# Kernel optimization log

Hardware: AMD Instinct MI355X
Metric: run time of the kernel (lower is better)

Reference implementation:

```python
import jax, jax.numpy as jnp
import numpy as np

B, M, D = 4, 2048, 1024


def setup_inputs() -> dict:
    key = jax.random.key(0)
    k1, k2, k3, k4 = jax.random.split(key, 4)
    x = jax.random.normal(k1, (B, M, D), dtype=jnp.float32)
    scale = 0.02
    wq = jax.random.normal(k2, (D, D), dtype=jnp.float32) * scale
    wk = jax.random.normal(k3, (D, D), dtype=jnp.float32) * scale
    wv = jax.random.normal(k4, (D, D), dtype=jnp.float32) * scale
    return {"x": x, "wq": wq, "wk": wk, "wv": wv}


def _rope_tables(m, d):
    # Faithful to source: phi = 10000 ** (-2*(i-1)/d)  (note the (i-1), incl. i=0)
    i = jnp.arange(d // 2, dtype=jnp.float32)
    phi = jnp.power(10000.0, -2.0 * (i - 1.0) / d)  # [d/2]
    pos = jnp.arange(m, dtype=jnp.float32)
    ang = pos[:, None] * phi[None, :]  # [m, d/2]
    return jnp.cos(ang), jnp.sin(ang)


def _apply_rope(t, cos, sin):
    # Original does t[pos] @ R[pos] (row-vector times rotation matrix):
    #   out_even =  t_even*cos + t_odd*sin
    #   out_odd  = -t_even*sin + t_odd*cos
    te = t[..., 0::2]  # [b, m, d/2]
    to = t[..., 1::2]
    oe = te * cos + to * sin
    oo = -te * sin + to * cos
    return jnp.stack([oe, oo], axis=-1).reshape(t.shape)


def reference(x, wq, wk, wv):
    b, m, d = x.shape
    q = x @ wq.T
    k = x @ wk.T
    v = x @ wv.T
    cos, sin = _rope_tables(m, d)
    qr = _apply_rope(q, cos, sin)
    kr = _apply_rope(k, cos, sin)
    # causal SDPA (dropout disabled for deterministic reference)
    scores = jnp.einsum('bqd,bkd->bqk', qr, kr) / jnp.sqrt(jnp.float32(d))
    causal = jnp.tril(jnp.ones((m, m), dtype=bool))
    scores = jnp.where(causal[None, :, :], scores, jnp.finfo(scores.dtype).min)
    attn = jax.nn.softmax(scores, axis=-1)
    return jnp.einsum('bqk,bkd->bqd', attn, v)
```

## Files before the change

### kernel.cpp

```cpp
#include <hip/hip_runtime.h>
#include <hip/hip_bf16.h>
#include <math.h>


typedef __bf16 bf16x8 __attribute__((ext_vector_type(8)));
typedef float  f32x4  __attribute__((ext_vector_type(4)));

__device__ __forceinline__ ushort f2bf(float f) {
    __hip_bfloat16 h = __float2bfloat16(f);
    return *reinterpret_cast<ushort*>(&h);
}

__device__ __forceinline__ void async_load16(const ushort* g, ushort* l) {
    __builtin_amdgcn_global_load_lds(
        (const __attribute__((address_space(1))) void*)g,
        (__attribute__((address_space(3))) void*)l, 16, 0, 0);
}

__global__ __launch_bounds__(256) void cvt_all_kernel(
    const float* __restrict__ x,  const float* __restrict__ wq,
    const float* __restrict__ wk, const float* __restrict__ wv,
    ushort* __restrict__ xb, ushort* __restrict__ wqb,
    ushort* __restrict__ wkb, ushort* __restrict__ wvb,
    float2* __restrict__ cs)
{
    const int t = blockIdx.y;
    if (t == 4) {
        const int idx = blockIdx.x * 256 + threadIdx.x;
        if (idx < 2048 * 512) {
            const int pos = idx >> 9, i = idx & 511;
            const float phi = powf(10000.0f, -2.0f * ((float)i - 1.0f) / 1024.0f);
            float s, c;
            sincosf((float)pos * phi, &s, &c);
            cs[idx] = make_float2(c, s);
        }
        return;
    }
    const float* in  = (t == 0) ? x  : (t == 1) ? wq  : (t == 2) ? wk  : wv;
    ushort*      out = (t == 0) ? xb : (t == 1) ? wqb : (t == 2) ? wkb : wvb;
    const int n4 = (t == 0) ? 2097152 : 262144;
    int i = blockIdx.x * blockDim.x + threadIdx.x;
    if (i < n4) {
        float4 f = ((const float4*)in)[i];
        ushort4 o;
        o.x = f2bf(f.x); o.y = f2bf(f.y); o.z = f2bf(f.z); o.w = f2bf(f.w);
        ((ushort4*)out)[i] = o;
    }
}

__device__ __forceinline__ void gemm128_core_sb64(
    const ushort* __restrict__ A, const ushort* __restrict__ B,
    int lda, int ldb, int m0, int n0, int kIters,
    ushort* As, ushort* Bs, f32x4 acc[4][4])
{
    const int tid  = threadIdx.x;
    const int lane = tid & 63, wave = tid >> 6;
    const int wm = (wave >> 1) * 64, wn = (wave & 1) * 64;
    const int quad = lane >> 4, l16 = lane & 15;
    const int srow8 = lane >> 3;
    const int gchk  = (lane & 7) ^ srow8;
    const ushort* ag = A + (size_t)(m0 + wave * 32 + srow8) * lda + gchk * 8;
    const ushort* bg = B + (size_t)(n0 + wave * 32 + srow8) * ldb + gchk * 8;
    const int p0 = quad ^ (l16 & 7);

    for (int kt = 0; kt < kIters; ++kt) {
        const int k0 = kt * 64;
#pragma unroll
        for (int s = 0; s < 4; ++s) {
            async_load16(ag + k0 + (size_t)(s * 8) * lda,
                         As + (wave * 32 + s * 8) * 64);
            async_load16(bg + k0 + (size_t)(s * 8) * ldb,
                         Bs + (wave * 32 + s * 8) * 64);
        }
        __syncthreads();
#pragma unroll
        for (int kk = 0; kk < 2; ++kk) {
            const int poff = (p0 ^ (kk << 2)) * 8;
            bf16x8 aF[4], bF[4];
#pragma unroll
            for (int i = 0; i < 4; ++i)
                aF[i] = *(const bf16x8*)(As + (wm + i * 16 + l16) * 64 + poff);
#pragma unroll
            for (int j = 0; j < 4; ++j)
                bF[j] = *(const bf16x8*)(Bs + (wn + j * 16 + l16) * 64 + poff);
#pragma unroll
            for (int i = 0; i < 4; ++i)
#pragma unroll
                for (int j = 0; j < 4; ++j)
                    acc[i][j] = __builtin_amdgcn_mfma_f32_16x16x32_bf16(aF[i], bF[j], acc[i][j], 0, 0, 0);
        }
        __syncthreads();
    }
}

__device__ __forceinline__ void gemm128_core_db64(
    const ushort* __restrict__ A, const ushort* __restrict__ B,
    int lda, int ldb, int m0, int n0, int kIters,
    ushort* As, ushort* Bs, f32x4 acc[4][4])
{
    const int tid  = threadIdx.x;
    const int lane = tid & 63, wave = tid >> 6;
    const int wm = (wave >> 1) * 64, wn = (wave & 1) * 64;
    const int quad = lane >> 4, l16 = lane & 15;
    const int srow8 = lane >> 3;
    const int gchk  = (lane & 7) ^ srow8;
    const ushort* ag = A + (size_t)(m0 + wave * 32 + srow8) * lda + gchk * 8;
    const ushort* bg = B + (size_t)(n0 + wave * 32 + srow8) * ldb + gchk * 8;
    const int p0 = quad ^ (l16 & 7);

#define STAGE64(K0, NB) do {                                            \
        _Pragma("unroll")                                               \
        for (int s = 0; s < 4; ++s) {                                   \
            async_load16(ag + (K0) + (size_t)(s * 8) * lda,             \
                         As + (NB) + (wave * 32 + s * 8) * 64);         \
            async_load16(bg + (K0) + (size_t)(s * 8) * ldb,             \
                         Bs + (NB) + (wave * 32 + s * 8) * 64);         \
        }                                                               \
    } while (0)

    STAGE64(0, 0);
    __syncthreads();

    int cur = 0;
    for (int kt = 0; kt < kIters; ++kt) {
        if (kt + 1 < kIters) STAGE64((kt + 1) * 64, (cur ^ 1) * 8192);
        const ushort* as = As + cur * 8192;
        const ushort* bs = Bs + cur * 8192;
#pragma unroll
        for (int kk = 0; kk < 2; ++kk) {
            const int poff = (p0 ^ (kk << 2)) * 8;
            bf16x8 aF[4], bF[4];
#pragma unroll
            for (int i = 0; i < 4; ++i)
                aF[i] = *(const bf16x8*)(as + (wm + i * 16 + l16) * 64 + poff);
#pragma unroll
            for (int j = 0; j < 4; ++j)
                bF[j] = *(const bf16x8*)(bs + (wn + j * 16 + l16) * 64 + poff);
#pragma unroll
            for (int i = 0; i < 4; ++i)
#pragma unroll
                for (int j = 0; j < 4; ++j)
                    acc[i][j] = __builtin_amdgcn_mfma_f32_16x16x32_bf16(aF[i], bF[j], acc[i][j], 0, 0, 0);
        }
        __syncthreads();
        cur ^= 1;
    }
#undef STAGE64
}

#define ACC_INIT4(acc) \
    _Pragma("unroll") for (int i = 0; i < 4; ++i) \
    _Pragma("unroll") for (int j = 0; j < 4; ++j) \
    _Pragma("unroll") for (int r = 0; r < 4; ++r) acc[i][j][r] = 0.0f;

__global__ __launch_bounds__(256) void qkv_rope_kernel(
    const ushort* __restrict__ xb, const ushort* __restrict__ wq,
    const ushort* __restrict__ wk, const ushort* __restrict__ wv,
    const float2* __restrict__ cs,
    ushort* __restrict__ Qr, ushort* __restrict__ Kr, ushort* __restrict__ VT)
{
    __shared__ __attribute__((aligned(16))) ushort As[128 * 64];
    __shared__ __attribute__((aligned(16))) ushort Bs[128 * 64];
    const int m0 = blockIdx.x * 128;
    const int n0 = blockIdx.y * 128;
    const int z  = blockIdx.z;
    const ushort* W = (z == 0) ? wq : (z == 1) ? wk : wv;

    f32x4 acc[4][4];
    ACC_INIT4(acc)
    gemm128_core_sb64(xb, W, 1024, 1024, m0, n0, 16, As, Bs, acc);

    const int lane = threadIdx.x & 63, wave = threadIdx.x >> 6;
    const int wm = (wave >> 1) * 64, wn = (wave & 1) * 64;
    const int quad = lane >> 4, l16 = lane & 15;

    if (z < 2) {
        ushort* out = (z == 0) ? Qr : Kr;
#pragma unroll
        for (int j = 0; j < 4; ++j) {
            const int n = n0 + wn + j * 16 + l16;
            const int iidx = n >> 1;
            const bool odd = n & 1;
#pragma unroll
            for (int i = 0; i < 4; ++i) {
                const int mbase = m0 + wm + i * 16 + quad * 4;
                const int pos0  = mbase & 2047;
                const float2* csp = cs + (size_t)pos0 * 512 + iidx;
#pragma unroll
                for (int r = 0; r < 4; ++r) {
                    const float2 sc = csp[(size_t)r * 512];
                    float v = acc[i][j][r];
                    float p = __shfl_xor(v, 1);
                    float o = odd ? (v * sc.x - p * sc.y) : (v * sc.x + p * sc.y);
                    out[(size_t)(mbase + r) * 1024 + n] = f2bf(o);
                }
            }
        }
    } else {
#pragma unroll
        for (int i = 0; i < 4; ++i) {
            const int mbase = m0 + wm + i * 16 + quad * 4;
            const int b = mbase >> 11, pos0 = mbase & 2047;
#pragma unroll
            for (int j = 0; j < 4; ++j) {
                const int n = n0 + wn + j * 16 + l16;
                ushort4 o;
                o.x = f2bf(acc[i][j][0]); o.y = f2bf(acc[i][j][1]);
                o.z = f2bf(acc[i][j][2]); o.w = f2bf(acc[i][j][3]);
                *(ushort4*)(VT + ((size_t)b * 1024 + n) * 2048 + pos0) = o;
            }
        }
    }
}

__global__ __launch_bounds__(256) void scores_kernel(
    const ushort* __restrict__ Qr, const ushort* __restrict__ Kr,
    float* __restrict__ S)
{
    const int m0 = blockIdx.x * 128;
    const int n0 = blockIdx.y * 128;
    if (n0 > m0 + 127) return;
    const int b = blockIdx.z;
    __shared__ __attribute__((aligned(16))) ushort As[2 * 128 * 64];
    __shared__ __attribute__((aligned(16))) ushort Bs[2 * 128 * 64];
    const ushort* A = Qr + (size_t)b * 2048 * 1024;
    const ushort* B = Kr + (size_t)b * 2048 * 1024;
    float* Sb = S + (size_t)b * 2048 * 2048;

    f32x4 acc[4][4];
    ACC_INIT4(acc)
    gemm128_core_db64(A, B, 1024, 1024, m0, n0, 16, As, Bs, acc);

    const int lane = threadIdx.x & 63, wave = threadIdx.x >> 6;
    const int wm = (wave >> 1) * 64, wn = (wave & 1) * 64;
    const int quad = lane >> 4, l16 = lane & 15;
#pragma unroll
    for (int i = 0; i < 4; ++i)
#pragma unroll
        for (int j = 0; j < 4; ++j) {
            const int n = n0 + wn + j * 16 + l16;
#pragma unroll
            for (int r = 0; r < 4; ++r) {
                const int m = m0 + wm + i * 16 + quad * 4 + r;
                Sb[(size_t)m * 2048 + n] = acc[i][j][r] * 0.03125f;
            }
        }
}

__global__ __launch_bounds__(256) void softmax_kernel(
    const float* __restrict__ S, ushort* __restrict__ P)
{
    __shared__ float red[4];
    const int row = blockIdx.x, tid = threadIdx.x, b = blockIdx.y;
    const int lane = tid & 63, wave = tid >> 6;
    const float* s = S + ((size_t)b * 2048 + row) * 2048;
    ushort*      p = P + ((size_t)b * 2048 + row) * 2048;
    const int nvalid = row + 1;
    const int wlimit = (row & ~127) + 128;
    const int j0 = tid * 8;

    float v[8] = {0.0f, 0.0f, 0.0f, 0.0f, 0.0f, 0.0f, 0.0f, 0.0f};
    if (j0 < nvalid) {
        float4 f0 = *(const float4*)(s + j0);
        v[0]=f0.x; v[1]=f0.y; v[2]=f0.z; v[3]=f0.w;
    }
    if (j0 + 4 < nvalid) {
        float4 f1 = *(const float4*)(s + j0 + 4);
        v[4]=f1.x; v[5]=f1.y; v[6]=f1.z; v[7]=f1.w;
    }

    float mx = -3.402823466e38f;
#pragma unroll
    for (int u = 0; u < 8; ++u) if (j0 + u < nvalid) mx = fmaxf(mx, v[u]);
#pragma unroll
    for (int d = 1; d < 64; d <<= 1) mx = fmaxf(mx, __shfl_xor(mx, d));
    if (lane == 0) red[wave] = mx;
    __syncthreads();
    mx = fmaxf(fmaxf(red[0], red[1]), fmaxf(red[2], red[3]));

    float sum = 0.0f;
#pragma unroll
    for (int u = 0; u < 8; ++u) {
        v[u] = (j0 + u < nvalid) ? __expf(v[u] - mx) : 0.0f;
        sum += v[u];
    }
#pragma unroll
    for (int d = 1; d < 64; d <<= 1) sum += __shfl_xor(sum, d);
    __syncthreads();
    if (lane == 0) red[wave] = sum;
    __syncthreads();
    const float inv = 1.0f / (red[0] + red[1] + red[2] + red[3]);

    if (j0 < wlimit) {
        ushort o[8];
#pragma unroll
        for (int u = 0; u < 8; ++u) o[u] = f2bf(v[u] * inv);
        *(int4*)(p + j0) = *(const int4*)o;
    }
}

__global__ __launch_bounds__(256) void pv_kernel(
    const ushort* __restrict__ P, const ushort* __restrict__ VT,
    float* __restrict__ out)
{
    __shared__ __attribute__((aligned(16))) ushort As[2 * 128 * 64];
    __shared__ __attribute__((aligned(16))) ushort Bs[2 * 128 * 64];
    const int x  = blockIdx.x;
    const int mt = (x & 1) ? (15 - (x >> 1)) : (x >> 1);
    const int m0 = mt * 128;
    const int n0 = blockIdx.y * 128;
    const int b  = blockIdx.z;
    const ushort* A = P + (size_t)b * 2048 * 2048;
    const ushort* B = VT + (size_t)b * 1024 * 2048;
    const int kIters = (m0 + 128) / 64;

    f32x4 acc[4][4];
    ACC_INIT4(acc)
    gemm128_core_db64(A, B, 2048, 2048, m0, n0, kIters, As, Bs, acc);

    const int lane = threadIdx.x & 63, wave = threadIdx.x >> 6;
    const int wm = (wave >> 1) * 64, wn = (wave & 1) * 64;
    const int quad = lane >> 4, l16 = lane & 15;
#pragma unroll
    for (int i = 0; i < 4; ++i)
#pragma unroll
        for (int j = 0; j < 4; ++j) {
            const int n = n0 + wn + j * 16 + l16;
#pragma unroll
            for (int r = 0; r < 4; ++r) {
                const int m = m0 + wm + i * 16 + quad * 4 + r;
                out[((size_t)b * 2048 + m) * 1024 + n] = acc[i][j][r];
            }
        }
}

extern "C" void kernel_launch(void* const* d_in, const int* in_sizes, int n_in,
                              void* d_out, int out_size, void* d_ws, size_t ws_size,
                              hipStream_t stream) {
    const float* x  = (const float*)d_in[0];
    const float* wq = (const float*)d_in[1];
    const float* wk = (const float*)d_in[2];
    const float* wv = (const float*)d_in[3];

    const size_t MiB = 1024 * 1024;
    char* ws = (char*)d_ws;
    ushort* xb  = (ushort*)(ws);
    ushort* wqb = (ushort*)(ws +  16 * MiB);
    ushort* wkb = (ushort*)(ws +  18 * MiB);
    ushort* wvb = (ushort*)(ws +  20 * MiB);
    ushort* Qr  = (ushort*)(ws +  22 * MiB);
    ushort* Kr  = (ushort*)(ws +  38 * MiB);
    ushort* VT  = (ushort*)(ws +  54 * MiB);
    float*  S   = (float* )(ws +  70 * MiB);
    ushort* P   = (ushort*)(ws + 134 * MiB);
    float2* cs  = (float2*)(ws + 166 * MiB);
    float*  out = (float*)d_out;

    cvt_all_kernel <<<dim3(8192, 5),   256, 0, stream>>>(x, wq, wk, wv, xb, wqb, wkb, wvb, cs);
    qkv_rope_kernel<<<dim3(64, 8, 3),  256, 0, stream>>>(xb, wqb, wkb, wvb, cs, Qr, Kr, VT);
    scores_kernel  <<<dim3(16, 16, 4), 256, 0, stream>>>(Qr, Kr, S);
    softmax_kernel <<<dim3(2048, 4),   256, 0, stream>>>(S, P);
    pv_kernel      <<<dim3(16, 8, 4),  256, 0, stream>>>(P, VT, out);
}
```

Before: 258.5 us.

## Enlarge QKV projection tile to 256x256 with 512-thread blocks

Rewrites the QKV+RoPE projection GEMM to use 256x256 output tiles computed by 8 waves, each holding a 128x64 sub-tile (8x4 MFMA accumulators), instead of 128x128 tiles with 4 waves. This raises arithmetic intensity per LDS load and cuts global re-reads of x and the weights. The grid drops from 1536 to 384 blocks, which may underfill the GPU's CUs, and doubled accumulator registers plus 64KB LDS lower occupancy. The unused single-buffer helper is removed.

```diff
diff --git a/kernel.cpp b/kernel.cpp
--- a/kernel.cpp
+++ b/kernel.cpp
@@ -48,7 +48,7 @@
     }
 }
 
-__device__ __forceinline__ void gemm128_core_sb64(
+__device__ __forceinline__ void gemm128_core_db64(
     const ushort* __restrict__ A, const ushort* __restrict__ B,
     int lda, int ldb, int m0, int n0, int kIters,
     ushort* As, ushort* Bs, f32x4 acc[4][4])
@@ -63,51 +63,6 @@
     const ushort* bg = B + (size_t)(n0 + wave * 32 + srow8) * ldb + gchk * 8;
     const int p0 = quad ^ (l16 & 7);
 
-    for (int kt = 0; kt < kIters; ++kt) {
-        const int k0 = kt * 64;
-#pragma unroll
-        for (int s = 0; s < 4; ++s) {
-            async_load16(ag + k0 + (size_t)(s * 8) * lda,
-                         As + (wave * 32 + s * 8) * 64);
-            async_load16(bg + k0 + (size_t)(s * 8) * ldb,
-                         Bs + (wave * 32 + s * 8) * 64);
-        }
-        __syncthreads();
-#pragma unroll
-        for (int kk = 0; kk < 2; ++kk) {
-            const int poff = (p0 ^ (kk << 2)) * 8;
-            bf16x8 aF[4], bF[4];
-#pragma unroll
-            for (int i = 0; i < 4; ++i)
-                aF[i] = *(const bf16x8*)(As + (wm + i * 16 + l16) * 64 + poff);
-#pragma unroll
-            for (int j = 0; j < 4; ++j)
-                bF[j] = *(const bf16x8*)(Bs + (wn + j * 16 + l16) * 64 + poff);
-#pragma unroll
-            for (int i = 0; i < 4; ++i)
-#pragma unroll
-                for (int j = 0; j < 4; ++j)
-                    acc[i][j] = __builtin_amdgcn_mfma_f32_16x16x32_bf16(aF[i], bF[j], acc[i][j], 0, 0, 0);
-        }
-        __syncthreads();
-    }
-}
-
-__device__ __forceinline__ void gemm128_core_db64(
-    const ushort* __restrict__ A, const ushort* __restrict__ B,
-    int lda, int ldb, int m0, int n0, int kIters,
-    ushort* As, ushort* Bs, f32x4 acc[4][4])
-{
-    const int tid  = threadIdx.x;
-    const int lane = tid & 63, wave = tid >> 6;
-    const int wm = (wave >> 1) * 64, wn = (wave & 1) * 64;
-    const int quad = lane >> 4, l16 = lane & 15;
-    const int srow8 = lane >> 3;
-    const int gchk  = (lane & 7) ^ srow8;
-    const ushort* ag = A + (size_t)(m0 + wave * 32 + srow8) * lda + gchk * 8;
-    const ushort* bg = B + (size_t)(n0 + wave * 32 + srow8) * ldb + gchk * 8;
-    const int p0 = quad ^ (l16 & 7);
-
 #define STAGE64(K0, NB) do {                                            \
         _Pragma("unroll")                                               \
         for (int s = 0; s < 4; ++s) {                                   \
@@ -153,26 +108,66 @@
     _Pragma("unroll") for (int j = 0; j < 4; ++j) \
     _Pragma("unroll") for (int r = 0; r < 4; ++r) acc[i][j][r] = 0.0f;
 
-__global__ __launch_bounds__(256) void qkv_rope_kernel(
+__global__ __launch_bounds__(512) void qkv_rope_kernel(
     const ushort* __restrict__ xb, const ushort* __restrict__ wq,
     const ushort* __restrict__ wk, const ushort* __restrict__ wv,
     const float2* __restrict__ cs,
     ushort* __restrict__ Qr, ushort* __restrict__ Kr, ushort* __restrict__ VT)
 {
-    __shared__ __attribute__((aligned(16))) ushort As[128 * 64];
-    __shared__ __attribute__((aligned(16))) ushort Bs[128 * 64];
-    const int m0 = blockIdx.x * 128;
-    const int n0 = blockIdx.y * 128;
+    __shared__ __attribute__((aligned(16))) ushort As[256 * 64];
+    __shared__ __attribute__((aligned(16))) ushort Bs[256 * 64];
+    const int m0 = blockIdx.x * 256;
+    const int n0 = blockIdx.y * 256;
     const int z  = blockIdx.z;
     const ushort* W = (z == 0) ? wq : (z == 1) ? wk : wv;
 
-    f32x4 acc[4][4];
-    ACC_INIT4(acc)
-    gemm128_core_sb64(xb, W, 1024, 1024, m0, n0, 16, As, Bs, acc);
-
-    const int lane = threadIdx.x & 63, wave = threadIdx.x >> 6;
-    const int wm = (wave >> 1) * 64, wn = (wave & 1) * 64;
+    const int tid  = threadIdx.x;
+    const int lane = tid & 63, wave = tid >> 6;
+    const int wm = (wave >> 2) * 128;
+    const int wn = (wave & 3) * 64;
     const int quad = lane >> 4, l16 = lane & 15;
+    const int srow8 = lane >> 3;
+    const int gchk  = (lane & 7) ^ srow8;
+    const ushort* ag = xb + (size_t)(m0 + wave * 32 + srow8) * 1024 + gchk * 8;
+    const ushort* bg = W  + (size_t)(n0 + wave * 32 + srow8) * 1024 + gchk * 8;
+    const int p0 = quad ^ (l16 & 7);
+
+    f32x4 acc[8][4];
+#pragma unroll
+    for (int i = 0; i < 8; ++i)
+#pragma unroll
+        for (int j = 0; j < 4; ++j)
+#pragma unroll
+            for (int r = 0; r < 4; ++r) acc[i][j][r] = 0.0f;
+
+    for (int kt = 0; kt < 16; ++kt) {
+        const int k0 = kt * 64;
+#pragma unroll
+        for (int s = 0; s < 4; ++s) {
+            async_load16(ag + k0 + (size_t)(s * 8) * 1024,
+                         As + (wave * 32 + s * 8) * 64);
+            async_load16(bg + k0 + (size_t)(s * 8) * 1024,
+                         Bs + (wave * 32 + s * 8) * 64);
+        }
+        __syncthreads();
+#pragma unroll
+        for (int kk = 0; kk < 2; ++kk) {
+            const int poff = (p0 ^ (kk << 2)) * 8;
+            bf16x8 aF[8], bF[4];
+#pragma unroll
+            for (int i = 0; i < 8; ++i)
+                aF[i] = *(const bf16x8*)(As + (wm + i * 16 + l16) * 64 + poff);
+#pragma unroll
+            for (int j = 0; j < 4; ++j)
+                bF[j] = *(const bf16x8*)(Bs + (wn + j * 16 + l16) * 64 + poff);
+#pragma unroll
+            for (int i = 0; i < 8; ++i)
+#pragma unroll
+                for (int j = 0; j < 4; ++j)
+                    acc[i][j] = __builtin_amdgcn_mfma_f32_16x16x32_bf16(aF[i], bF[j], acc[i][j], 0, 0, 0);
+        }
+        __syncthreads();
+    }
 
     if (z < 2) {
         ushort* out = (z == 0) ? Qr : Kr;
@@ -182,7 +177,7 @@
             const int iidx = n >> 1;
             const bool odd = n & 1;
 #pragma unroll
-            for (int i = 0; i < 4; ++i) {
+            for (int i = 0; i < 8; ++i) {
                 const int mbase = m0 + wm + i * 16 + quad * 4;
                 const int pos0  = mbase & 2047;
                 const float2* csp = cs + (size_t)pos0 * 512 + iidx;
@@ -198,7 +193,7 @@
         }
     } else {
 #pragma unroll
-        for (int i = 0; i < 4; ++i) {
+        for (int i = 0; i < 8; ++i) {
             const int mbase = m0 + wm + i * 16 + quad * 4;
             const int b = mbase >> 11, pos0 = mbase & 2047;
 #pragma unroll
@@ -357,7 +352,7 @@
     float*  out = (float*)d_out;
 
     cvt_all_kernel <<<dim3(8192, 5),   256, 0, stream>>>(x, wq, wk, wv, xb, wqb, wkb, wvb, cs);
-    qkv_rope_kernel<<<dim3(64, 8, 3),  256, 0, stream>>>(xb, wqb, wkb, wvb, cs, Qr, Kr, VT);
+    qkv_rope_kernel<<<dim3(32, 4, 3),  512, 0, stream>>>(xb, wqb, wkb, wvb, cs, Qr, Kr, VT);
     scores_kernel  <<<dim3(16, 16, 4), 256, 0, stream>>>(Qr, Kr, S);
     softmax_kernel <<<dim3(2048, 4),   256, 0, stream>>>(S, P);
     pv_kernel      <<<dim3(16, 8, 4),  256, 0, stream>>>(P, VT, out);
```

After: 270.3 us. 1.05x slower.

## Split-K the scores GEMM into two halves summed in softmax

Applied to the files above, without the earlier changes.

The QK^T scores kernel now splits the 1024-wide reduction into two 512-wide halves, each written to its own fp32 score buffer, which doubles the number of blocks for better CU occupancy. It also switches to a single-buffered GEMM core with smaller shared memory. The softmax kernel reads both partial buffers and adds them. This costs an extra 64 MiB scores buffer write and read, plus the loss of double-buffered load overlap in the GEMM.

```diff
diff --git a/kernel.cpp b/kernel.cpp
--- a/kernel.cpp
+++ b/kernel.cpp
@@ -215,21 +215,22 @@
 
 __global__ __launch_bounds__(256) void scores_kernel(
     const ushort* __restrict__ Qr, const ushort* __restrict__ Kr,
-    float* __restrict__ S)
+    float* __restrict__ S1, float* __restrict__ S2)
 {
     const int m0 = blockIdx.x * 128;
     const int n0 = blockIdx.y * 128;
     if (n0 > m0 + 127) return;
-    const int b = blockIdx.z;
-    __shared__ __attribute__((aligned(16))) ushort As[2 * 128 * 64];
-    __shared__ __attribute__((aligned(16))) ushort Bs[2 * 128 * 64];
-    const ushort* A = Qr + (size_t)b * 2048 * 1024;
-    const ushort* B = Kr + (size_t)b * 2048 * 1024;
-    float* Sb = S + (size_t)b * 2048 * 2048;
+    const int b = blockIdx.z >> 1;
+    const int h = blockIdx.z & 1;
+    __shared__ __attribute__((aligned(16))) ushort As[128 * 64];
+    __shared__ __attribute__((aligned(16))) ushort Bs[128 * 64];
+    const ushort* A = Qr + (size_t)b * 2048 * 1024 + h * 512;
+    const ushort* B = Kr + (size_t)b * 2048 * 1024 + h * 512;
+    float* Sb = (h ? S2 : S1) + (size_t)b * 2048 * 2048;
 
     f32x4 acc[4][4];
     ACC_INIT4(acc)
-    gemm128_core_db64(A, B, 1024, 1024, m0, n0, 16, As, Bs, acc);
+    gemm128_core_sb64(A, B, 1024, 1024, m0, n0, 8, As, Bs, acc);
 
     const int lane = threadIdx.x & 63, wave = threadIdx.x >> 6;
     const int wm = (wave >> 1) * 64, wn = (wave & 1) * 64;
@@ -248,25 +249,29 @@
 }
 
 __global__ __launch_bounds__(256) void softmax_kernel(
-    const float* __restrict__ S, ushort* __restrict__ P)
+    const float* __restrict__ S1, const float* __restrict__ S2,
+    ushort* __restrict__ P)
 {
     __shared__ float red[4];
     const int row = blockIdx.x, tid = threadIdx.x, b = blockIdx.y;
     const int lane = tid & 63, wave = tid >> 6;
-    const float* s = S + ((size_t)b * 2048 + row) * 2048;
-    ushort*      p = P + ((size_t)b * 2048 + row) * 2048;
+    const float* s1 = S1 + ((size_t)b * 2048 + row) * 2048;
+    const float* s2 = S2 + ((size_t)b * 2048 + row) * 2048;
+    ushort*      p  = P  + ((size_t)b * 2048 + row) * 2048;
     const int nvalid = row + 1;
     const int wlimit = (row & ~127) + 128;
     const int j0 = tid * 8;
 
     float v[8] = {0.0f, 0.0f, 0.0f, 0.0f, 0.0f, 0.0f, 0.0f, 0.0f};
     if (j0 < nvalid) {
-        float4 f0 = *(const float4*)(s + j0);
-        v[0]=f0.x; v[1]=f0.y; v[2]=f0.z; v[3]=f0.w;
+        float4 a = *(const float4*)(s1 + j0);
+        float4 c = *(const float4*)(s2 + j0);
+        v[0]=a.x+c.x; v[1]=a.y+c.y; v[2]=a.z+c.z; v[3]=a.w+c.w;
     }
     if (j0 + 4 < nvalid) {
-        float4 f1 = *(const float4*)(s + j0 + 4);
-        v[4]=f1.x; v[5]=f1.y; v[6]=f1.z; v[7]=f1.w;
+        float4 a = *(const float4*)(s1 + j0 + 4);
+        float4 c = *(const float4*)(s2 + j0 + 4);
+        v[4]=a.x+c.x; v[5]=a.y+c.y; v[6]=a.z+c.z; v[7]=a.w+c.w;
     }
 
     float mx = -3.402823466e38f;
@@ -351,14 +356,15 @@
     ushort* Qr  = (ushort*)(ws +  22 * MiB);
     ushort* Kr  = (ushort*)(ws +  38 * MiB);
     ushort* VT  = (ushort*)(ws +  54 * MiB);
-    float*  S   = (float* )(ws +  70 * MiB);
+    float*  S1  = (float* )(ws +  70 * MiB);
     ushort* P   = (ushort*)(ws + 134 * MiB);
     float2* cs  = (float2*)(ws + 166 * MiB);
+    float*  S2  = (float* )(ws + 174 * MiB);
     float*  out = (float*)d_out;
 
     cvt_all_kernel <<<dim3(8192, 5),   256, 0, stream>>>(x, wq, wk, wv, xb, wqb, wkb, wvb, cs);
     qkv_rope_kernel<<<dim3(64, 8, 3),  256, 0, stream>>>(xb, wqb, wkb, wvb, cs, Qr, Kr, VT);
-    scores_kernel  <<<dim3(16, 16, 4), 256, 0, stream>>>(Qr, Kr, S);
-    softmax_kernel <<<dim3(2048, 4),   256, 0, stream>>>(S, P);
+    scores_kernel  <<<dim3(16, 16, 8), 256, 0, stream>>>(Qr, Kr, S1, S2);
+    softmax_kernel <<<dim3(2048, 4),   256, 0, stream>>>(S1, S2, P);
     pv_kernel      <<<dim3(16, 8, 4),  256, 0, stream>>>(P, VT, out);
 }
```

After: 270.5 us. +4.6%, slower.
